# Performance work log

Measured on AMD Instinct MI355X. Metric: run time of the kernel, lower is better.

## Reference

```python
import jax, jax.numpy as jnp
import numpy as np
from jax import lax

SCALE = 2
K_UP = 5


def conv2d(x, w, pad):
    return lax.conv_general_dilated(
        x, w, window_strides=(1, 1), padding=[(pad, pad), (pad, pad)],
        dimension_numbers=("NCHW", "OIHW", "NCHW"))


def bn(x, gamma, beta, mean, var, eps=1e-5):
    # eval-mode batchnorm, per-channel (NCHW)
    inv = gamma / jnp.sqrt(var + eps)
    return x * inv[None, :, None, None] + (beta - mean * inv)[None, :, None, None]


def pixel_shuffle(x, r):
    b, crr, h, w = x.shape
    c = crr // (r * r)
    x = x.reshape(b, c, r, r, h, w)
    x = x.transpose(0, 1, 4, 2, 5, 3)  # b, c, h, r, w, r
    return x.reshape(b, c, h * r, w * r)


def setup_inputs():
    key = jax.random.key(0)
    k0, k1, k2 = jax.random.split(key, 3)
    b, c, h, w = 2, 256, 64, 64
    cmid, cenc = 64, (SCALE * K_UP) ** 2  # 64, 100
    return {
        "X": jax.random.normal(k0, (b, c, h, w), jnp.float32),
        "comp_w": jax.random.normal(k1, (cmid, c, 1, 1), jnp.float32) * 0.05,
        "comp_gamma": jnp.ones((cmid,), jnp.float32),
        "comp_beta": jnp.zeros((cmid,), jnp.float32),
        "comp_mean": jnp.zeros((cmid,), jnp.float32),
        "comp_var": jnp.ones((cmid,), jnp.float32),
        "enc_w": jax.random.normal(k2, (cenc, cmid, 3, 3), jnp.float32) * 0.05,
        "enc_gamma": jnp.ones((cenc,), jnp.float32),
        "enc_beta": jnp.zeros((cenc,), jnp.float32),
        "enc_mean": jnp.zeros((cenc,), jnp.float32),
        "enc_var": jnp.ones((cenc,), jnp.float32),
        "power_p": jnp.ones((1,), jnp.float32),
    }


def reference(X, comp_w, comp_gamma, comp_beta, comp_mean, comp_var,
              enc_w, enc_gamma, enc_beta, enc_mean, enc_var, power_p):
    b, c, h, w = X.shape
    h_, w_ = h * SCALE, w * SCALE

    # kernel prediction branch
    W = conv2d(X, comp_w, 0)
    W = jax.nn.relu(bn(W, comp_gamma, comp_beta, comp_mean, comp_var))
    W = conv2d(W, enc_w, 1)
    W = bn(W, enc_gamma, enc_beta, enc_mean, enc_var)  # no relu
    W = pixel_shuffle(W, SCALE)  # (b, k_up^2, h_, w_)

    # power-normalized softmax: W = softmax(clamp(W)^clamp(p)) over taps
    i = jnp.clip(power_p, 1e-5)  # PowerIndex -> learnable scalar exponent
    W = jnp.clip(W, 1e-5)
    W = jnp.power(W, i[0])
    W = jax.nn.softmax(W, axis=1)

    # content branch: nearest upsample then dilated unfold (k=5, dil=2, pad=4)
    Xu = jnp.repeat(jnp.repeat(X, SCALE, axis=2), SCALE, axis=3)  # (b,c,h_,w_)
    pad = (K_UP // 2) * SCALE  # 4
    Xp = jnp.pad(Xu, ((0, 0), (0, 0), (pad, pad), (pad, pad)))
    patches = jnp.stack(
        [Xp[:, :, ki * SCALE: ki * SCALE + h_, kj * SCALE: kj * SCALE + w_]
         for ki in range(K_UP) for kj in range(K_UP)], axis=2)  # (b,c,25,h_,w_)

    return jnp.einsum("bkhw,bckhw->bchw", W, patches)
```

## Files before the change

### kernel.cpp

```cpp
#include <hip/hip_runtime.h>
#include <math.h>

#define NPX 4096
#define H2 128
#define W2 128
#define PP 66

__global__ __launch_bounds__(256) void k1_conv1x1(
    const float* __restrict__ X, const float* __restrict__ w,
    const float* __restrict__ g, const float* __restrict__ bt,
    const float* __restrict__ m, const float* __restrict__ var,
    float* __restrict__ mid_p)
{
    __shared__ float red[3 * 4 * 64];
    int tid = threadIdx.x;
    int x = tid & 63;
    int ciq = __builtin_amdgcn_readfirstlane(tid >> 6);
    int bx = blockIdx.x;
    int bb = bx >> 6, y = bx & 63;
    int co0 = blockIdx.y * 4;
    int ci0 = ciq * 64;

    const float* xp = X + ((size_t)(bb * 256 + ci0)) * NPX + y * 64 + x;
    const float* wp = w + (size_t)co0 * 256 + ci0;

    float acc[4] = {0.f, 0.f, 0.f, 0.f};

    #pragma unroll 8
    for (int ci = 0; ci < 64; ++ci) {
        float xv = xp[(size_t)ci * NPX];
        #pragma unroll
        for (int j = 0; j < 4; ++j)
            acc[j] += xv * wp[j * 256 + ci];
    }

    if (ciq > 0) {
        #pragma unroll
        for (int j = 0; j < 4; ++j)
            red[((ciq - 1) * 4 + j) * 64 + x] = acc[j];
    }
    __syncthreads();
    if (ciq == 0) {
        #pragma unroll
        for (int j = 0; j < 4; ++j) {
            float a = acc[j] + red[(0 * 4 + j) * 64 + x]
                             + red[(1 * 4 + j) * 64 + x]
                             + red[(2 * 4 + j) * 64 + x];
            int co = co0 + j;
            float inv = g[co] * rsqrtf(var[co] + 1e-5f);
            a = fmaxf(a * inv + (bt[co] - m[co] * inv), 0.f);
            mid_p[((size_t)(bb * 64 + co) * PP + (y + 1)) * PP + (x + 1)] = a;
        }
    }
}

__global__ __launch_bounds__(256) void k2a_conv3x3(
    const float* __restrict__ mid_p, const float* __restrict__ ew,
    float* __restrict__ enc)
{
    __shared__ float red[3 * 10 * 64];
    int tid = threadIdx.x;
    int x = tid & 63;
    int ciq = __builtin_amdgcn_readfirstlane(tid >> 6);
    int bx = blockIdx.x;
    int bb = bx >> 6, y = bx & 63;
    int co0 = blockIdx.y * 10;

    float acc[10];
    #pragma unroll
    for (int j = 0; j < 10; ++j) acc[j] = 0.f;

    const float* wb = ew + ((size_t)co0 * 64 + ciq * 16) * 9;

    #pragma unroll 2
    for (int ci = 0; ci < 16; ++ci) {
        const float* P = mid_p + (((size_t)(bb * 64 + ciq * 16 + ci)) * PP + y) * PP + x;
        float v0 = P[0],       v1 = P[1],          v2 = P[2];
        float v3 = P[PP],      v4 = P[PP + 1],     v5 = P[PP + 2];
        float v6 = P[2 * PP],  v7 = P[2 * PP + 1], v8 = P[2 * PP + 2];
        const float* wp = wb + ci * 9;
        #pragma unroll
        for (int j = 0; j < 10; ++j) {
            const float* wj = wp + j * 576;
            acc[j] += v0 * wj[0] + v1 * wj[1] + v2 * wj[2]
                    + v3 * wj[3] + v4 * wj[4] + v5 * wj[5]
                    + v6 * wj[6] + v7 * wj[7] + v8 * wj[8];
        }
    }

    if (ciq > 0) {
        #pragma unroll
        for (int j = 0; j < 10; ++j)
            red[((ciq - 1) * 10 + j) * 64 + x] = acc[j];
    }
    __syncthreads();
    if (ciq == 0) {
        #pragma unroll
        for (int j = 0; j < 10; ++j) {
            float a = acc[j] + red[(0 * 10 + j) * 64 + x]
                             + red[(1 * 10 + j) * 64 + x]
                             + red[(2 * 10 + j) * 64 + x];
            enc[((size_t)bb * 100 + co0 + j) * NPX + y * 64 + x] = a;
        }
    }
}

__global__ __launch_bounds__(64) void k2b_softmax(
    const float* __restrict__ enc,
    const float* __restrict__ g, const float* __restrict__ bt,
    const float* __restrict__ m, const float* __restrict__ var,
    const float* __restrict__ power_p,
    float* __restrict__ wn)
{
    int s = blockIdx.x & 3;
    int p = (blockIdx.x >> 2) * 64 + threadIdx.x;
    int bb = p >> 12, sp = p & (NPX - 1);
    float pw = fmaxf(power_p[0], 1e-5f);
    float tv[25];
    float mx = -1e30f;
    #pragma unroll
    for (int k = 0; k < 25; ++k) {
        int co = 4 * k + s;
        float inv = g[co] * rsqrtf(var[co] + 1e-5f);
        float e = enc[((size_t)bb * 100 + co) * NPX + sp] * inv + (bt[co] - m[co] * inv);
        e = fmaxf(e, 1e-5f);
        float xq = exp2f(pw * log2f(e));
        tv[k] = xq;
        mx = fmaxf(mx, xq);
    }
    float sum = 0.f;
    #pragma unroll
    for (int k = 0; k < 25; ++k) {
        float e = expf(tv[k] - mx);
        tv[k] = e;
        sum += e;
    }
    float r = 1.0f / sum;
    #pragma unroll
    for (int k = 0; k < 25; ++k)
        wn[((size_t)bb * 100 + s * 25 + k) * NPX + sp] = tv[k] * r;
}

__global__ __launch_bounds__(256) void k3_carafe(
    const float* __restrict__ X, const float* __restrict__ wn,
    float* __restrict__ out)
{
    __shared__ float xt[16 * 5 * 72];
    int tid = threadIdx.x;
    int px = tid & 63;
    int bx = blockIdx.x;
    int bb = bx >> 6, y = bx & 63;
    int c0 = blockIdx.y * 16;

    for (int idx = tid; idx < 5760; idx += 256) {
        int ch = idx / 360;
        int rem = idx - ch * 360;
        int r = rem / 72, c = rem - r * 72;
        int gy = y + r - 2, gx = c - 2;
        float val = 0.f;
        if (c < 68 && (unsigned)gy < 64u && (unsigned)gx < 64u)
            val = X[((size_t)(bb * 256 + c0 + ch)) * NPX + gy * 64 + gx];
        xt[idx] = val;
    }
    __syncthreads();

    int wq = __builtin_amdgcn_readfirstlane(tid >> 6);

    float a[4][4];
    #pragma unroll
    for (int i = 0; i < 4; ++i)
        #pragma unroll
        for (int j = 0; j < 4; ++j) a[i][j] = 0.f;

    const float* wbase = wn + ((size_t)bb * 100) * NPX + y * 64 + px;
    const float* xbase = xt + wq * 4 * 360 + px;

    #pragma unroll 1
    for (int ki = 0; ki < 5; ++ki) {
        #pragma unroll
        for (int kj = 0; kj < 5; ++kj) {
            int k = ki * 5 + kj;
            float w0 = wbase[(size_t)(k)      * NPX];
            float w1 = wbase[(size_t)(25 + k) * NPX];
            float w2 = wbase[(size_t)(50 + k) * NPX];
            float w3 = wbase[(size_t)(75 + k) * NPX];
            #pragma unroll
            for (int cc = 0; cc < 4; ++cc) {
                float v = xbase[cc * 360 + ki * 72 + kj];
                a[cc][0] += w0 * v;
                a[cc][1] += w1 * v;
                a[cc][2] += w2 * v;
                a[cc][3] += w3 * v;
            }
        }
    }

    #pragma unroll
    for (int cc = 0; cc < 4; ++cc) {
        int ch = wq * 4 + cc;
        float* ob = out + ((size_t)(bb * 256 + c0 + ch) * H2 + 2 * y) * W2 + 2 * px;
        ((float2*)ob)[0]        = make_float2(a[cc][0], a[cc][1]);
        ((float2*)(ob + W2))[0] = make_float2(a[cc][2], a[cc][3]);
    }
}

extern "C" void kernel_launch(void* const* d_in, const int* in_sizes, int n_in,
                              void* d_out, int out_size, void* d_ws, size_t ws_size,
                              hipStream_t stream)
{
    const float* X  = (const float*)d_in[0];
    const float* cw = (const float*)d_in[1];
    const float* cg = (const float*)d_in[2];
    const float* cb = (const float*)d_in[3];
    const float* cm = (const float*)d_in[4];
    const float* cv = (const float*)d_in[5];
    const float* ew = (const float*)d_in[6];
    const float* eg = (const float*)d_in[7];
    const float* eb = (const float*)d_in[8];
    const float* em = (const float*)d_in[9];
    const float* ev = (const float*)d_in[10];
    const float* pp = (const float*)d_in[11];
    float* out = (float*)d_out;

    float* ws   = (float*)d_ws;
    float* midp = ws;
    float* enc  = ws + 557568;
    float* wn   = ws + 557568 + 819200;

    hipMemsetAsync(midp, 0, 557568 * sizeof(float), stream);
    k1_conv1x1<<<dim3(128, 16), 256, 0, stream>>>(X, cw, cg, cb, cm, cv, midp);
    k2a_conv3x3<<<dim3(128, 10), 256, 0, stream>>>(midp, ew, enc);
    k2b_softmax<<<dim3(512), 64, 0, stream>>>(enc, eg, eb, em, ev, pp, wn);
    k3_carafe<<<dim3(128, 16), 256, 0, stream>>>(X, wn, out);
}
```

Baseline: 153.2 us.

## Fuse 3x3 conv with power-softmax and write padding borders in conv1x1

The 3x3 encoder conv and the power-normalized softmax become one kernel. Each block computes all 25 taps for one subpixel group, so the intermediate enc buffer is never written to or read from global memory. The memset of the padded mid buffer is replaced by having the 1x1 conv kernel write the zero borders itself. This removes two launches and a round trip through global memory, but the grid drops from 1280 to 512 blocks and each thread now holds 25 accumulators, which lowers parallelism and raises register pressure.

```diff
diff --git a/kernel.cpp b/kernel.cpp
--- a/kernel.cpp
+++ b/kernel.cpp
@@ -49,30 +49,46 @@
             int co = co0 + j;
             float inv = g[co] * rsqrtf(var[co] + 1e-5f);
             a = fmaxf(a * inv + (bt[co] - m[co] * inv), 0.f);
-            mid_p[((size_t)(bb * 64 + co) * PP + (y + 1)) * PP + (x + 1)] = a;
-        }
-    }
-}
-
-__global__ __launch_bounds__(256) void k2a_conv3x3(
+            float* pl = mid_p + (size_t)(bb * 64 + co) * PP * PP;
+            pl[(size_t)(y + 1) * PP + (x + 1)] = a;
+            if (x == 0) {
+                pl[(size_t)(y + 1) * PP] = 0.f;
+                pl[(size_t)(y + 1) * PP + 65] = 0.f;
+            }
+            if (y == 0) {
+                pl[x] = 0.f;
+                pl[(size_t)65 * PP + x] = 0.f;
+                if (x < 2) {
+                    pl[64 + x] = 0.f;
+                    pl[(size_t)65 * PP + 64 + x] = 0.f;
+                }
+            }
+        }
+    }
+}
+
+__global__ __launch_bounds__(256) void k2_fused(
     const float* __restrict__ mid_p, const float* __restrict__ ew,
-    float* __restrict__ enc)
-{
-    __shared__ float red[3 * 10 * 64];
+    const float* __restrict__ g, const float* __restrict__ bt,
+    const float* __restrict__ m, const float* __restrict__ var,
+    const float* __restrict__ power_p,
+    float* __restrict__ wn)
+{
+    __shared__ float red[3 * 25 * 64];
     int tid = threadIdx.x;
     int x = tid & 63;
     int ciq = __builtin_amdgcn_readfirstlane(tid >> 6);
     int bx = blockIdx.x;
     int bb = bx >> 6, y = bx & 63;
-    int co0 = blockIdx.y * 10;
-
-    float acc[10];
+    int s = blockIdx.y;
+
+    float acc[25];
     #pragma unroll
-    for (int j = 0; j < 10; ++j) acc[j] = 0.f;
-
-    const float* wb = ew + ((size_t)co0 * 64 + ciq * 16) * 9;
-
-    #pragma unroll 2
+    for (int k = 0; k < 25; ++k) acc[k] = 0.f;
+
+    const float* wb = ew + ((size_t)s * 64 + ciq * 16) * 9;
+
+    #pragma unroll 1
     for (int ci = 0; ci < 16; ++ci) {
         const float* P = mid_p + (((size_t)(bb * 64 + ciq * 16 + ci)) * PP + y) * PP + x;
         float v0 = P[0],       v1 = P[1],          v2 = P[2];
@@ -80,9 +96,9 @@
         float v6 = P[2 * PP],  v7 = P[2 * PP + 1], v8 = P[2 * PP + 2];
         const float* wp = wb + ci * 9;
         #pragma unroll
-        for (int j = 0; j < 10; ++j) {
-            const float* wj = wp + j * 576;
-            acc[j] += v0 * wj[0] + v1 * wj[1] + v2 * wj[2]
+        for (int k = 0; k < 25; ++k) {
+            const float* wj = wp + (size_t)k * 4 * 576;
+            acc[k] += v0 * wj[0] + v1 * wj[1] + v2 * wj[2]
                     + v3 * wj[3] + v4 * wj[4] + v5 * wj[5]
                     + v6 * wj[6] + v7 * wj[7] + v8 * wj[8];
         }
@@ -90,55 +106,39 @@
 
     if (ciq > 0) {
         #pragma unroll
-        for (int j = 0; j < 10; ++j)
-            red[((ciq - 1) * 10 + j) * 64 + x] = acc[j];
+        for (int k = 0; k < 25; ++k)
+            red[((ciq - 1) * 25 + k) * 64 + x] = acc[k];
     }
     __syncthreads();
     if (ciq == 0) {
-        #pragma unroll
-        for (int j = 0; j < 10; ++j) {
-            float a = acc[j] + red[(0 * 10 + j) * 64 + x]
-                             + red[(1 * 10 + j) * 64 + x]
-                             + red[(2 * 10 + j) * 64 + x];
-            enc[((size_t)bb * 100 + co0 + j) * NPX + y * 64 + x] = a;
-        }
-    }
-}
-
-__global__ __launch_bounds__(64) void k2b_softmax(
-    const float* __restrict__ enc,
-    const float* __restrict__ g, const float* __restrict__ bt,
-    const float* __restrict__ m, const float* __restrict__ var,
-    const float* __restrict__ power_p,
-    float* __restrict__ wn)
-{
-    int s = blockIdx.x & 3;
-    int p = (blockIdx.x >> 2) * 64 + threadIdx.x;
-    int bb = p >> 12, sp = p & (NPX - 1);
-    float pw = fmaxf(power_p[0], 1e-5f);
-    float tv[25];
-    float mx = -1e30f;
-    #pragma unroll
-    for (int k = 0; k < 25; ++k) {
-        int co = 4 * k + s;
-        float inv = g[co] * rsqrtf(var[co] + 1e-5f);
-        float e = enc[((size_t)bb * 100 + co) * NPX + sp] * inv + (bt[co] - m[co] * inv);
-        e = fmaxf(e, 1e-5f);
-        float xq = exp2f(pw * log2f(e));
-        tv[k] = xq;
-        mx = fmaxf(mx, xq);
-    }
-    float sum = 0.f;
-    #pragma unroll
-    for (int k = 0; k < 25; ++k) {
-        float e = expf(tv[k] - mx);
-        tv[k] = e;
-        sum += e;
-    }
-    float r = 1.0f / sum;
-    #pragma unroll
-    for (int k = 0; k < 25; ++k)
-        wn[((size_t)bb * 100 + s * 25 + k) * NPX + sp] = tv[k] * r;
+        float pw = fmaxf(power_p[0], 1e-5f);
+        float tv[25];
+        float mx = -1e30f;
+        #pragma unroll
+        for (int k = 0; k < 25; ++k) {
+            float a = acc[k] + red[(0 * 25 + k) * 64 + x]
+                             + red[(1 * 25 + k) * 64 + x]
+                             + red[(2 * 25 + k) * 64 + x];
+            int co = 4 * k + s;
+            float inv = g[co] * rsqrtf(var[co] + 1e-5f);
+            float e = a * inv + (bt[co] - m[co] * inv);
+            e = fmaxf(e, 1e-5f);
+            float xq = exp2f(pw * log2f(e));
+            tv[k] = xq;
+            mx = fmaxf(mx, xq);
+        }
+        float sum = 0.f;
+        #pragma unroll
+        for (int k = 0; k < 25; ++k) {
+            float e = expf(tv[k] - mx);
+            tv[k] = e;
+            sum += e;
+        }
+        float r = 1.0f / sum;
+        #pragma unroll
+        for (int k = 0; k < 25; ++k)
+            wn[((size_t)bb * 100 + s * 25 + k) * NPX + y * 64 + x] = tv[k] * r;
+    }
 }
 
 __global__ __launch_bounds__(256) void k3_carafe(
@@ -224,12 +224,9 @@
 
     float* ws   = (float*)d_ws;
     float* midp = ws;
-    float* enc  = ws + 557568;
-    float* wn   = ws + 557568 + 819200;
-
-    hipMemsetAsync(midp, 0, 557568 * sizeof(float), stream);
+    float* wn   = ws + 557568;
+
     k1_conv1x1<<<dim3(128, 16), 256, 0, stream>>>(X, cw, cg, cb, cm, cv, midp);
-    k2a_conv3x3<<<dim3(128, 10), 256, 0, stream>>>(midp, ew, enc);
-    k2b_softmax<<<dim3(512), 64, 0, stream>>>(enc, eg, eb, em, ev, pp, wn);
+    k2_fused<<<dim3(128, 4), 256, 0, stream>>>(midp, ew, eg, eb, em, ev, pp, wn);
     k3_carafe<<<dim3(128, 16), 256, 0, stream>>>(X, wn, out);
 }
```

Result: slower. 172.2 us (+12.4%).
